# Kernel optimization log

Hardware: AMD Instinct MI355X
Metric: run time of the kernel (lower is better)

## Reference

```python
import jax, jax.numpy as jnp
import numpy as np


def _grid_sample_bilinear(img, gx, gy):
    """Bilinear sampling at pixel coords (gx, gy), align_corners=True convention,
    zero padding for out-of-bounds (matches old-default torch grid_sample).
    img: [B,C,H,W]; gx, gy: [B,H,W] in pixel units."""
    B, C, H, W = img.shape
    x0 = jnp.floor(gx)
    y0 = jnp.floor(gy)
    x1 = x0 + 1.0
    y1 = y0 + 1.0
    wx1 = gx - x0
    wx0 = 1.0 - wx1
    wy1 = gy - y0
    wy0 = 1.0 - wy1
    img_flat = img.reshape(B, C, H * W)

    def corner(xc, yc, w):
        valid = ((xc >= 0) & (xc <= W - 1) & (yc >= 0) & (yc <= H - 1)).astype(img.dtype)
        xi = jnp.clip(xc, 0, W - 1).astype(jnp.int32)
        yi = jnp.clip(yc, 0, H - 1).astype(jnp.int32)
        idx = (yi * W + xi).reshape(B, 1, H * W)  # broadcast over C
        vals = jnp.take_along_axis(img_flat, idx, axis=2).reshape(B, C, H, W)
        return vals * (w * valid)[:, None, :, :]

    return (corner(x0, y0, wx0 * wy0) + corner(x1, y0, wx1 * wy0)
            + corner(x0, y1, wx0 * wy1) + corner(x1, y1, wx1 * wy1))


def _warp(image, flo):
    B, C, H, W = image.shape
    # base grid in pixel coords; torch normalizes 2*v/(W-1)-1 then grid_sample
    # (align_corners=True) de-normalizes back to pixel coords -> they cancel.
    xx = jnp.arange(W, dtype=image.dtype)[None, None, :]   # [1,1,W]
    yy = jnp.arange(H, dtype=image.dtype)[None, :, None]   # [1,H,1]
    gx = xx + flo[:, 0]  # [B,H,W]
    gy = yy + flo[:, 1]
    out = _grid_sample_bilinear(image, gx, gy)
    # mask = grid_sample(ones) then hard threshold; values are channel-independent
    ones = jnp.ones((B, 1, H, W), dtype=image.dtype)
    mask = _grid_sample_bilinear(ones, gx, gy)
    mask = jnp.where(mask < 0.9999, jnp.zeros((), image.dtype), jnp.ones((), image.dtype))
    return out * mask


def setup_inputs() -> dict:
    key = jax.random.key(0)
    k1, k2 = jax.random.split(key)
    B, C, H, W = 8, 16, 512, 512
    image = jax.random.normal(k1, (B, C, H, W), dtype=jnp.float32)
    # realistic flow magnitudes of a few pixels
    UVgrid = jax.random.normal(k2, (B, 2, H, W), dtype=jnp.float32) * 8.0
    return {"image": image, "UVgrid": UVgrid}


def reference(image, UVgrid):
    # scale=1, upsampleMode='nearest': Upsample to [H*1, W*1] is identity,
    # UVgrid * scale is identity.
    return _warp(image, UVgrid)
```

## Files before the change

### kernel.cpp

```cpp
#include <hip/hip_runtime.h>

#define BATCH 8
#define CH    16
#define HH    512
#define WW    512
#define HW    (HH * WW)

#define TILE  32
#define RPAD  16
#define REGE  64
#define NPX   4


typedef __attribute__((address_space(1))) const void global_cvoid;
typedef __attribute__((address_space(3))) void lds_void;

__device__ __forceinline__ void gll16(const float* g, float* l) {
    __builtin_amdgcn_global_load_lds((global_cvoid*)g, (lds_void*)l, 16, 0, 0);
}

#define WAITVM(n) asm volatile("s_waitcnt vmcnt(" #n ")" ::: "memory")
#define BAR()     __builtin_amdgcn_s_barrier()

#define STAGE(g, nb) do {                                               \
    const float* pc_ = img + ib + (size_t)(g) * HW;                     \
    _Pragma("unroll")                                                   \
    for (int k_ = 0; k_ < 4; ++k_) {                                    \
        gll16(pc_ + goff[k_], &buf[nb][(k_ * 4 + wv) * 4][0]);          \
    }                                                                   \
} while (0)

#define GATHER(g, cb) do {                                              \
    const float* pl_ = &buf[cb][0][0];                                  \
    _Pragma("unroll")                                                   \
    for (int p_ = 0; p_ < NPX; ++p_) {                                  \
        const int l_   = lidx[p_];                                      \
        const int dx_  = dxv[p_];                                       \
        const int dyo_ = dyov[p_];                                      \
        const float v00 = pl_[l_];                                      \
        const float v01 = pl_[l_ + dx_];                                \
        const float v10 = pl_[l_ + dyo_];                               \
        const float v11 = pl_[l_ + dx_ + dyo_];                         \
        res[g][p_] = w00[p_]*v00 + w01[p_]*v01                          \
                   + w10[p_]*v10 + w11[p_]*v11;                         \
    }                                                                   \
} while (0)

#define PHASE(g) do {                                                   \
    GATHER(g, (g) % 3);                                                 \
    WAITVM(4);                                                          \
    BAR();                                                              \
    STAGE((g) + 3, (g) % 3);                                            \
} while (0)

__global__ __launch_bounds__(256, 3) void warp_cnt(
    const float* __restrict__ img,
    const float* __restrict__ flo,
    float* __restrict__ out)
{
    __shared__ float buf[3][REGE][REGE];

    const int t   = threadIdx.x;
    const int bid = blockIdx.x;
    const int tile = (bid & 7) * 256 + (bid >> 3);
    const int b    = tile >> 8;
    const int ty   = (tile >> 4) & 15;
    const int tx   = tile & 15;
    const int xb   = tx * TILE;
    const int yb   = ty * TILE;
    const int x0r  = xb - RPAD;
    const int y0r  = yb - RPAD;

    const int lane = t & 63;
    const int wv   = t >> 6;
    const int sub  = lane >> 4;
    const int xch  = x0r + (lane & 15) * 4;
    const size_t ib = (size_t)b * CH * HW;

    int goff[4];
#pragma unroll
    for (int k = 0; k < 4; ++k) {
        const int q  = k * 4 + wv;
        const int ry = q * 4 + sub;
        const int gy = min(max(y0r + ry, 0), HH - 1);
        goff[k] = min(max(gy * WW + xch, 0), HW - 4);
    }

    const float* fbp = flo + (size_t)b * 2 * HW;
    float fxv[NPX], fyv[NPX];
#pragma unroll
    for (int p = 0; p < NPX; ++p) {
        const int pix = p * 256 + t;
        const int hw  = (yb + (pix >> 5)) * WW + xb + (pix & 31);
        fxv[p] = fbp[hw];
        fyv[p] = fbp[HW + hw];
    }
    asm volatile("" ::: "memory");

    STAGE(0, 0);
    STAGE(1, 1);
    STAGE(2, 2);

    float w00[NPX], w01[NPX], w10[NPX], w11[NPX];
    int   lidx[NPX], dxv[NPX], dyov[NPX], obase[NPX];
    int   fbmask = 0;

#pragma unroll
    for (int p = 0; p < NPX; ++p) {
        const int pix = p * 256 + t;
        const int row = pix >> 5;
        const int col = pix & 31;
        const int h   = yb + row;
        const int w   = xb + col;
        obase[p] = h * WW + w;

        const float gx = (float)w + fxv[p];
        const float gy = (float)h + fyv[p];

        const float x0f = floorf(gx), y0f = floorf(gy);
        const float wx1 = gx - x0f, wx0 = 1.0f - wx1;
        const float wy1 = gy - y0f, wy0 = 1.0f - wy1;

        const bool vx0 = (x0f >= 0.0f)        && (x0f <= (float)(WW - 1));
        const bool vx1 = (x0f + 1.0f >= 0.0f) && (x0f + 1.0f <= (float)(WW - 1));
        const bool vy0 = (y0f >= 0.0f)        && (y0f <= (float)(HH - 1));
        const bool vy1 = (y0f + 1.0f >= 0.0f) && (y0f + 1.0f <= (float)(HH - 1));

        float a00 = wx0 * wy0 * ((vx0 && vy0) ? 1.0f : 0.0f);
        float a01 = wx1 * wy0 * ((vx1 && vy0) ? 1.0f : 0.0f);
        float a10 = wx0 * wy1 * ((vx0 && vy1) ? 1.0f : 0.0f);
        float a11 = wx1 * wy1 * ((vx1 && vy1) ? 1.0f : 0.0f);

        const float msum = a00 + a01 + a10 + a11;
        const float mask = (msum < 0.9999f) ? 0.0f : 1.0f;
        w00[p] = a00 * mask; w01[p] = a01 * mask;
        w10[p] = a10 * mask; w11[p] = a11 * mask;

        const int x0 = min(max((int)x0f, 0), WW - 1);
        const int x1 = min(max((int)x0f + 1, 0), WW - 1);
        const int y0 = min(max((int)y0f, 0), HH - 1);
        const int y1 = min(max((int)y0f + 1, 0), HH - 1);

        const int dx = x1 - x0;
        const int dy = y1 - y0;
        dxv[p]  = dx;
        dyov[p] = dy * REGE;

        const int xl = x0 - x0r;
        const int yl = y0 - y0r;
        if (!((xl >= 0) && (xl + dx <= REGE - 1) &&
              (yl >= 0) && (yl + dy <= REGE - 1)))
            fbmask |= (1 << p);
        lidx[p] = min(max(yl, 0), REGE - 2) * REGE + min(max(xl, 0), REGE - 2);
    }

    float res[CH][NPX];

    WAITVM(8);
    BAR();

    PHASE(0);   PHASE(1);   PHASE(2);   PHASE(3);
    PHASE(4);   PHASE(5);   PHASE(6);   PHASE(7);
    PHASE(8);   PHASE(9);   PHASE(10);  PHASE(11);
    PHASE(12);
    GATHER(13, 1);  WAITVM(4);  BAR();
    GATHER(14, 2);  WAITVM(0);  BAR();
    GATHER(15, 0);

#pragma unroll
    for (int c = 0; c < CH; ++c) {
        float* o0 = out + ib + (size_t)c * HW;
#pragma unroll
        for (int p = 0; p < NPX; ++p)
            o0[obase[p]] = res[c][p];
    }

    if (fbmask) {
#pragma unroll
        for (int p = 0; p < NPX; ++p) {
            if (!(fbmask & (1 << p))) continue;
            const int pix = p * 256 + t;
            const int row = pix >> 5;
            const int col = pix & 31;
            const int h   = yb + row;
            const int w   = xb + col;
            const int hw  = h * WW + w;

            const float gx = (float)w + fxv[p];
            const float gy = (float)h + fyv[p];

            const float x0f = floorf(gx), y0f = floorf(gy);
            const float wx1 = gx - x0f, wx0 = 1.0f - wx1;
            const float wy1 = gy - y0f, wy0 = 1.0f - wy1;

            const bool vx0 = (x0f >= 0.0f)        && (x0f <= (float)(WW - 1));
            const bool vx1 = (x0f + 1.0f >= 0.0f) && (x0f + 1.0f <= (float)(WW - 1));
            const bool vy0 = (y0f >= 0.0f)        && (y0f <= (float)(HH - 1));
            const bool vy1 = (y0f + 1.0f >= 0.0f) && (y0f + 1.0f <= (float)(HH - 1));

            float a00 = wx0 * wy0 * ((vx0 && vy0) ? 1.0f : 0.0f);
            float a01 = wx1 * wy0 * ((vx1 && vy0) ? 1.0f : 0.0f);
            float a10 = wx0 * wy1 * ((vx0 && vy1) ? 1.0f : 0.0f);
            float a11 = wx1 * wy1 * ((vx1 && vy1) ? 1.0f : 0.0f);

            const float msum = a00 + a01 + a10 + a11;
            const float mask = (msum < 0.9999f) ? 0.0f : 1.0f;
            a00 *= mask; a01 *= mask; a10 *= mask; a11 *= mask;

            const int x0 = min(max((int)x0f, 0), WW - 1);
            const int x1 = min(max((int)x0f + 1, 0), WW - 1);
            const int y0 = min(max((int)y0f, 0), HH - 1);
            const int y1 = min(max((int)y0f + 1, 0), HH - 1);

            const int gA  = y0 * WW + x0;
            const int dx  = x1 - x0;
            const int dyo = (y1 - y0) * WW;

            const float* ic = img + ib;
            float*       oc = out + ib + hw;
            for (int c = 0; c < CH; ++c) {
                const float* pc = ic + (size_t)c * HW;
                const float v = a00 * pc[gA]
                              + a01 * pc[gA + dx]
                              + a10 * pc[gA + dyo]
                              + a11 * pc[gA + dx + dyo];
                oc[(size_t)c * HW] = v;
            }
        }
    }
}

extern "C" void kernel_launch(void* const* d_in, const int* in_sizes, int n_in,
                              void* d_out, int out_size, void* d_ws, size_t ws_size,
                              hipStream_t stream) {
    const float* img = (const float*)d_in[0];
    const float* flo = (const float*)d_in[1];
    float* out = (float*)d_out;

    const int blocks = BATCH * (HH / TILE) * (WW / TILE);
    warp_cnt<<<blocks, 256, 0, stream>>>(img, flo, out);
}
```

Measured before the change: 280.3 us.

## Store each channel directly after gathering and fix neighbour offsets to constants

Each channel's bilinear result is now written to global memory right after it is gathered, instead of being held in a 16x4 register array until the end. Stores therefore overlap with later staging, and the vmcnt waits are raised to count the outstanding stores. Pixels whose clamped neighbours collapse (dx or dy equal to zero) now go to the fallback path, so the LDS gather can use the constant offsets +1 and +REGE. Sched barriers are added after each s_barrier to stop the compiler moving work across them. This cuts register pressure and offset arithmetic, but relies on the hand-tuned wait counts matching the outstanding loads and stores.

```diff
diff --git a/kernel.cpp b/kernel.cpp
--- a/kernel.cpp
+++ b/kernel.cpp
@@ -20,7 +20,8 @@
 }
 
 #define WAITVM(n) asm volatile("s_waitcnt vmcnt(" #n ")" ::: "memory")
-#define BAR()     __builtin_amdgcn_s_barrier()
+#define BAR()     do { __builtin_amdgcn_s_barrier();                    \
+                       __builtin_amdgcn_sched_barrier(0); } while (0)
 
 #define STAGE(g, nb) do {                                               \
     const float* pc_ = img + ib + (size_t)(g) * HW;                     \
@@ -30,30 +31,22 @@
     }                                                                   \
 } while (0)
 
-#define GATHER(g, cb) do {                                              \
+#define GATHERST(g, cb) do {                                            \
     const float* pl_ = &buf[cb][0][0];                                  \
+    float* o0_ = out + ib + (size_t)(g) * HW;                           \
     _Pragma("unroll")                                                   \
     for (int p_ = 0; p_ < NPX; ++p_) {                                  \
-        const int l_   = lidx[p_];                                      \
-        const int dx_  = dxv[p_];                                       \
-        const int dyo_ = dyov[p_];                                      \
+        const int l_ = lidx[p_];                                        \
         const float v00 = pl_[l_];                                      \
-        const float v01 = pl_[l_ + dx_];                                \
-        const float v10 = pl_[l_ + dyo_];                               \
-        const float v11 = pl_[l_ + dx_ + dyo_];                         \
-        res[g][p_] = w00[p_]*v00 + w01[p_]*v01                          \
-                   + w10[p_]*v10 + w11[p_]*v11;                         \
+        const float v01 = pl_[l_ + 1];                                  \
+        const float v10 = pl_[l_ + REGE];                               \
+        const float v11 = pl_[l_ + REGE + 1];                           \
+        o0_[obase[p_]] = w00[p_]*v00 + w01[p_]*v01                      \
+                       + w10[p_]*v10 + w11[p_]*v11;                     \
     }                                                                   \
 } while (0)
 
-#define PHASE(g) do {                                                   \
-    GATHER(g, (g) % 3);                                                 \
-    WAITVM(4);                                                          \
-    BAR();                                                              \
-    STAGE((g) + 3, (g) % 3);                                            \
-} while (0)
-
-__global__ __launch_bounds__(256, 3) void warp_cnt(
+__global__ __launch_bounds__(256, 3) void warp_ds2(
     const float* __restrict__ img,
     const float* __restrict__ flo,
     float* __restrict__ out)
@@ -102,7 +95,7 @@
     STAGE(2, 2);
 
     float w00[NPX], w01[NPX], w10[NPX], w11[NPX];
-    int   lidx[NPX], dxv[NPX], dyov[NPX], obase[NPX];
+    int   lidx[NPX], obase[NPX];
     int   fbmask = 0;
 
 #pragma unroll
@@ -143,37 +136,34 @@
 
         const int dx = x1 - x0;
         const int dy = y1 - y0;
-        dxv[p]  = dx;
-        dyov[p] = dy * REGE;
-
         const int xl = x0 - x0r;
         const int yl = y0 - y0r;
-        if (!((xl >= 0) && (xl + dx <= REGE - 1) &&
-              (yl >= 0) && (yl + dy <= REGE - 1)))
+
+        if (dx == 0 || dy == 0 ||
+            !((xl >= 0) && (xl <= REGE - 2) && (yl >= 0) && (yl <= REGE - 2)))
             fbmask |= (1 << p);
         lidx[p] = min(max(yl, 0), REGE - 2) * REGE + min(max(xl, 0), REGE - 2);
     }
 
-    float res[CH][NPX];
-
     WAITVM(8);
     BAR();
 
-    PHASE(0);   PHASE(1);   PHASE(2);   PHASE(3);
-    PHASE(4);   PHASE(5);   PHASE(6);   PHASE(7);
-    PHASE(8);   PHASE(9);   PHASE(10);  PHASE(11);
-    PHASE(12);
-    GATHER(13, 1);  WAITVM(4);  BAR();
-    GATHER(14, 2);  WAITVM(0);  BAR();
-    GATHER(15, 0);
-
-#pragma unroll
-    for (int c = 0; c < CH; ++c) {
-        float* o0 = out + ib + (size_t)c * HW;
-#pragma unroll
-        for (int p = 0; p < NPX; ++p)
-            o0[obase[p]] = res[c][p];
-    }
+    GATHERST(0, 0);   WAITVM(8);   BAR();  STAGE(3, 0);
+    GATHERST(1, 1);   WAITVM(12);  BAR();  STAGE(4, 1);
+    GATHERST(2, 2);   WAITVM(12);  BAR();  STAGE(5, 2);
+    GATHERST(3, 0);   WAITVM(12);  BAR();  STAGE(6, 0);
+    GATHERST(4, 1);   WAITVM(12);  BAR();  STAGE(7, 1);
+    GATHERST(5, 2);   WAITVM(12);  BAR();  STAGE(8, 2);
+    GATHERST(6, 0);   WAITVM(12);  BAR();  STAGE(9, 0);
+    GATHERST(7, 1);   WAITVM(12);  BAR();  STAGE(10, 1);
+    GATHERST(8, 2);   WAITVM(12);  BAR();  STAGE(11, 2);
+    GATHERST(9, 0);   WAITVM(12);  BAR();  STAGE(12, 0);
+    GATHERST(10, 1);  WAITVM(12);  BAR();  STAGE(13, 1);
+    GATHERST(11, 2);  WAITVM(12);  BAR();  STAGE(14, 2);
+    GATHERST(12, 0);  WAITVM(12);  BAR();  STAGE(15, 0);
+    GATHERST(13, 1);  WAITVM(12);  BAR();
+    GATHERST(14, 2);  WAITVM(8);   BAR();
+    GATHERST(15, 0);
 
     if (fbmask) {
 #pragma unroll
@@ -238,5 +228,5 @@
     float* out = (float*)d_out;
 
     const int blocks = BATCH * (HH / TILE) * (WW / TILE);
-    warp_cnt<<<blocks, 256, 0, stream>>>(img, flo, out);
+    warp_ds2<<<blocks, 256, 0, stream>>>(img, flo, out);
 }
```

Result: slower. 297.1 us (+6.0%).

## Use taller 32x64 tiles with 512 threads to cut halo overfetch

Applied to the files above, without the earlier changes.

Doubles the output tile height to 64 rows and the block to 512 threads. The staged LDS region grows from 64x64 to 96x64 per channel, which reduces redundant halo loading relative to useful pixels, from 4x to 3x overfetch. Staging loop counts and vmcnt waits are adjusted to the new per-thread load count. In exchange, LDS per block rises to 72KB, which limits how many blocks fit per CU, and the occupancy hint is changed to 4.

```diff
diff --git a/kernel.cpp b/kernel.cpp
--- a/kernel.cpp
+++ b/kernel.cpp
@@ -6,10 +6,13 @@
 #define WW    512
 #define HW    (HH * WW)
 
-#define TILE  32
+#define TILW  32
+#define TILH  64
 #define RPAD  16
-#define REGE  64
+#define REGW  64
+#define REGH  96
 #define NPX   4
+#define NTHR  512
 
 
 typedef __attribute__((address_space(1))) const void global_cvoid;
@@ -25,8 +28,8 @@
 #define STAGE(g, nb) do {                                               \
     const float* pc_ = img + ib + (size_t)(g) * HW;                     \
     _Pragma("unroll")                                                   \
-    for (int k_ = 0; k_ < 4; ++k_) {                                    \
-        gll16(pc_ + goff[k_], &buf[nb][(k_ * 4 + wv) * 4][0]);          \
+    for (int k_ = 0; k_ < 3; ++k_) {                                    \
+        gll16(pc_ + goff[k_], &buf[nb][(k_ * 8 + wv) * 4][0]);          \
     }                                                                   \
 } while (0)
 
@@ -48,26 +51,27 @@
 
 #define PHASE(g) do {                                                   \
     GATHER(g, (g) % 3);                                                 \
-    WAITVM(4);                                                          \
+    WAITVM(3);                                                          \
     BAR();                                                              \
     STAGE((g) + 3, (g) % 3);                                            \
 } while (0)
 
-__global__ __launch_bounds__(256, 3) void warp_cnt(
+__global__ __launch_bounds__(NTHR, 4) void warp_big(
     const float* __restrict__ img,
     const float* __restrict__ flo,
     float* __restrict__ out)
 {
-    __shared__ float buf[3][REGE][REGE];
+    __shared__ float buf[3][REGH][REGW];
 
     const int t   = threadIdx.x;
     const int bid = blockIdx.x;
-    const int tile = (bid & 7) * 256 + (bid >> 3);
-    const int b    = tile >> 8;
-    const int ty   = (tile >> 4) & 15;
-    const int tx   = tile & 15;
-    const int xb   = tx * TILE;
-    const int yb   = ty * TILE;
+    const int tile = (bid & 7) * 128 + (bid >> 3);
+    const int b    = tile >> 7;
+    const int ti   = tile & 127;
+    const int ty   = ti >> 4;
+    const int tx   = ti & 15;
+    const int xb   = tx * TILW;
+    const int yb   = ty * TILH;
     const int x0r  = xb - RPAD;
     const int y0r  = yb - RPAD;
 
@@ -77,10 +81,10 @@
     const int xch  = x0r + (lane & 15) * 4;
     const size_t ib = (size_t)b * CH * HW;
 
-    int goff[4];
-#pragma unroll
-    for (int k = 0; k < 4; ++k) {
-        const int q  = k * 4 + wv;
+    int goff[3];
+#pragma unroll
+    for (int k = 0; k < 3; ++k) {
+        const int q  = k * 8 + wv;
         const int ry = q * 4 + sub;
         const int gy = min(max(y0r + ry, 0), HH - 1);
         goff[k] = min(max(gy * WW + xch, 0), HW - 4);
@@ -90,7 +94,7 @@
     float fxv[NPX], fyv[NPX];
 #pragma unroll
     for (int p = 0; p < NPX; ++p) {
-        const int pix = p * 256 + t;
+        const int pix = p * NTHR + t;
         const int hw  = (yb + (pix >> 5)) * WW + xb + (pix & 31);
         fxv[p] = fbp[hw];
         fyv[p] = fbp[HW + hw];
@@ -107,7 +111,7 @@
 
 #pragma unroll
     for (int p = 0; p < NPX; ++p) {
-        const int pix = p * 256 + t;
+        const int pix = p * NTHR + t;
         const int row = pix >> 5;
         const int col = pix & 31;
         const int h   = yb + row;
@@ -144,26 +148,26 @@
         const int dx = x1 - x0;
         const int dy = y1 - y0;
         dxv[p]  = dx;
-        dyov[p] = dy * REGE;
+        dyov[p] = dy * REGW;
 
         const int xl = x0 - x0r;
         const int yl = y0 - y0r;
-        if (!((xl >= 0) && (xl + dx <= REGE - 1) &&
-              (yl >= 0) && (yl + dy <= REGE - 1)))
+        if (!((xl >= 0) && (xl + dx <= REGW - 1) &&
+              (yl >= 0) && (yl + dy <= REGH - 1)))
             fbmask |= (1 << p);
-        lidx[p] = min(max(yl, 0), REGE - 2) * REGE + min(max(xl, 0), REGE - 2);
+        lidx[p] = min(max(yl, 0), REGH - 2) * REGW + min(max(xl, 0), REGW - 2);
     }
 
     float res[CH][NPX];
 
-    WAITVM(8);
+    WAITVM(6);
     BAR();
 
     PHASE(0);   PHASE(1);   PHASE(2);   PHASE(3);
     PHASE(4);   PHASE(5);   PHASE(6);   PHASE(7);
     PHASE(8);   PHASE(9);   PHASE(10);  PHASE(11);
     PHASE(12);
-    GATHER(13, 1);  WAITVM(4);  BAR();
+    GATHER(13, 1);  WAITVM(3);  BAR();
     GATHER(14, 2);  WAITVM(0);  BAR();
     GATHER(15, 0);
 
@@ -179,7 +183,7 @@
 #pragma unroll
         for (int p = 0; p < NPX; ++p) {
             if (!(fbmask & (1 << p))) continue;
-            const int pix = p * 256 + t;
+            const int pix = p * NTHR + t;
             const int row = pix >> 5;
             const int col = pix & 31;
             const int h   = yb + row;
@@ -237,6 +241,6 @@
     const float* flo = (const float*)d_in[1];
     float* out = (float*)d_out;
 
-    const int blocks = BATCH * (HH / TILE) * (WW / TILE);
-    warp_cnt<<<blocks, 256, 0, stream>>>(img, flo, out);
+    const int blocks = BATCH * (WW / TILW) * (HH / TILH);
+    warp_big<<<blocks, NTHR, 0, stream>>>(img, flo, out);
 }
```

Result: faster. 269.9 us (-3.7%).
